# Kernel tuning notes

Measured on AMD Instinct MI355X. Metric: run time of the kernel, lower is better.

The kernel has to match this reference:

```python
import jax, jax.numpy as jnp
import numpy as np

N_EMBED = 512
E_DIM = 256
BETA = 0.25


def setup_inputs() -> dict:
    key = jax.random.key(0)
    k1, k2 = jax.random.split(key)
    z = jax.random.normal(k1, (32, 16, 16, 16, E_DIM), dtype=jnp.float32)
    embedding = jax.random.normal(k2, (N_EMBED, E_DIM), dtype=jnp.float32)
    return {"z": z, "embedding": embedding}


def reference(z, embedding):
    # Flatten spatial/batch dims: [N, e_dim]
    zf = z.reshape(-1, E_DIM)
    # similarity = ||z||^2 + ||e||^2 - 2 z.e  (squared distances)
    sim = (
        jnp.sum(zf * zf, axis=1, keepdims=True)
        + jnp.sum(embedding * embedding, axis=1)
        - 2.0 * jnp.einsum("bd,nd->bn", zf, embedding)
    )
    # NOTE: original code uses argmax (farthest code) -- faithfully reproduced.
    codebook_idxs = jnp.argmax(sim, axis=-1)
    # histogram side-effect: codebook_hist[idx] += 1
    hist = jnp.zeros((N_EMBED,), dtype=jnp.float32).at[codebook_idxs].add(1.0)
    z_q = embedding[codebook_idxs].reshape(z.shape)
    vq_loss = jnp.mean((z_q - jax.lax.stop_gradient(z)) ** 2)
    commitment_loss = BETA * jnp.mean((jax.lax.stop_gradient(z_q) - z) ** 2)
    # straight-through estimator
    z_q_st = z + jax.lax.stop_gradient(z_q - z)
    return (z_q_st, vq_loss, commitment_loss, codebook_idxs, hist)
```

## Files before the change

### kernel.cpp

```cpp
#include <hip/hip_runtime.h>
#include <hip/hip_bf16.h>

#define D 256
#define NC 512
#define NROWS 131072L

#define OFF_ZQ   0L
#define OFF_VQ   33554432L
#define OFF_CM   33554433L
#define OFF_IDX  33554434L
#define OFF_HIST 33685506L

#define WS_LPART 0
#define WS_HIST  2048
#define WS_E2    2560
#define WS_CNT   3072
#define WS_AMB   3136
#define WS_FIDX  134208
#define WS_BK    265280
#define WS_NEED  (330816L * 4)

#define MARGIN 1.25f

typedef __attribute__((ext_vector_type(8))) short bf16x8;
typedef __attribute__((ext_vector_type(4))) float f32x4;

#define AS1 __attribute__((address_space(1)))
#define AS3 __attribute__((address_space(3)))

__device__ __forceinline__ unsigned short f2bf(float f) {
    union { float f; unsigned int u; } a; a.f = f;
    return (unsigned short)((a.u + 0x7FFFu + ((a.u >> 16) & 1u)) >> 16);
}

__global__ void vq_init(float* __restrict__ ws) {
    int i = blockIdx.x * 1024 + threadIdx.x;
    if (i < 3073) ws[i] = 0.0f;
}

__global__ void vq_e2(const float* __restrict__ e, float* __restrict__ e2) {
    int c = blockIdx.x;
    int l = threadIdx.x;
    float4 v = *(const float4*)(e + c * D + l * 4);
    float s = v.x * v.x + v.y * v.y + v.z * v.z + v.w * v.w;
    #pragma unroll
    for (int off = 32; off; off >>= 1) s += __shfl_xor(s, off);
    if (l == 0) e2[c] = s;
}

__global__ void vq_convB(const float* __restrict__ e, unsigned short* __restrict__ Bk) {
    int code = blockIdx.x, k = threadIdx.x;
    unsigned short h = f2bf(e[code * D + k]);
    Bk[((k >> 5) * NC + code) * 32 + (k & 31)] = h;
}

__global__ __launch_bounds__(512, 4)
void vq_gemm(const float* __restrict__ z, const unsigned short* __restrict__ Bk,
             const float* __restrict__ e2, int* __restrict__ fidx,
             int* __restrict__ acnt, int* __restrict__ alist) {
    __shared__ __align__(16) unsigned short zh[64 * 264];
    __shared__ __align__(16) unsigned short Bs[512 * 32];
    __shared__ float red[64 * 4 * 3];

    const int tid = threadIdx.x;
    const int w = tid >> 6, l = tid & 63, q = l >> 4, ln = l & 15;
    const int wm = w >> 2, wn = w & 3;
    const long row0 = (long)blockIdx.x * 64;

    #pragma unroll
    for (int j = 0; j < 8; ++j) {
        int c = j * 512 + tid;
        int row = c >> 6, c4 = (c & 63) * 4;
        float4 av = *(const float4*)(z + (row0 + row) * D + c4);
        *(ushort4*)&zh[row * 264 + c4] =
            make_ushort4(f2bf(av.x), f2bf(av.y), f2bf(av.z), f2bf(av.w));
    }

    int bidx[8];
    #pragma unroll
    for (int nt = 0; nt < 8; ++nt) {
        int code = wn * 128 + nt * 16 + ln;
        int c = code * 4 + q;
        int d = c ^ ((code >> 1) & 3);
        bidx[nt] = d * 8;
    }

    f32x4 acc[2][8];
    #pragma unroll
    for (int mt = 0; mt < 2; ++mt)
        #pragma unroll
        for (int nt = 0; nt < 8; ++nt) acc[mt][nt] = (f32x4){0.f, 0.f, 0.f, 0.f};

    for (int s = 0; s < 8; ++s) {
        __syncthreads();
        const unsigned short* slabB = Bk + s * (NC * 32);
        #pragma unroll
        for (int j = 0; j < 4; ++j) {
            int dd = j * 512 + tid;
            int cc = dd ^ ((dd >> 3) & 3);
            __builtin_amdgcn_global_load_lds((const AS1 void*)(slabB + cc * 8),
                                             (AS3 void*)(Bs + dd * 8), 16, 0, 0);
        }
        __syncthreads();
        bf16x8 af[2], bfr[8];
        #pragma unroll
        for (int mt = 0; mt < 2; ++mt)
            af[mt] = *(const bf16x8*)&zh[(wm * 32 + mt * 16 + ln) * 264 + s * 32 + q * 8];
        #pragma unroll
        for (int nt = 0; nt < 8; ++nt)
            bfr[nt] = *(const bf16x8*)&Bs[bidx[nt]];
        #pragma unroll
        for (int mt = 0; mt < 2; ++mt)
            #pragma unroll
            for (int nt = 0; nt < 8; ++nt)
                acc[mt][nt] = __builtin_amdgcn_mfma_f32_16x16x32_bf16(af[mt], bfr[nt], acc[mt][nt], 0, 0, 0);
    }

    float e2v[8];
    #pragma unroll
    for (int nt = 0; nt < 8; ++nt) e2v[nt] = e2[wn * 128 + nt * 16 + ln];

    #pragma unroll
    for (int mt = 0; mt < 2; ++mt) {
        #pragma unroll
        for (int r = 0; r < 4; ++r) {
            float v1 = -3.0e38f, v2 = -3.0e38f; int i1 = 0;
            #pragma unroll
            for (int nt = 0; nt < 8; ++nt) {
                float v = e2v[nt] - 2.0f * acc[mt][nt][r];
                int c = wn * 128 + nt * 16 + ln;
                if (v > v1) { v2 = v1; v1 = v; i1 = c; }
                else if (v > v2) v2 = v;
            }
            #pragma unroll
            for (int off = 1; off < 16; off <<= 1) {
                float ov1 = __shfl_xor(v1, off);
                float ov2 = __shfl_xor(v2, off);
                int   oi1 = __shfl_xor(i1, off);
                if (ov1 > v1 || (ov1 == v1 && oi1 < i1)) {
                    v2 = fmaxf(v1, ov2); v1 = ov1; i1 = oi1;
                } else {
                    v2 = fmaxf(v2, ov1);
                }
            }
            if (ln == 0) {
                int rr = wm * 32 + mt * 16 + q * 4 + r;
                red[rr * 12 + wn * 3 + 0] = v1;
                red[rr * 12 + wn * 3 + 1] = (float)i1;
                red[rr * 12 + wn * 3 + 2] = v2;
            }
        }
    }
    __syncthreads();
    if (tid < 64) {
        float v1 = -3.0e38f, v2 = -3.0e38f; int i1 = 0;
        #pragma unroll
        for (int g = 0; g < 4; ++g) {
            float rv1 = red[tid * 12 + g * 3 + 0];
            int   ri  = (int)red[tid * 12 + g * 3 + 1];
            float rv2 = red[tid * 12 + g * 3 + 2];
            if (rv1 > v1) { v2 = fmaxf(v1, rv2); v1 = rv1; i1 = ri; }
            else v2 = fmaxf(v2, rv1);
        }
        fidx[row0 + tid] = i1;
        if (v1 - v2 < MARGIN) {
            int ppos = atomicAdd(acnt, 1);
            alist[ppos] = (int)(row0 + tid);
        }
    }
}

__global__ __launch_bounds__(256, 2)
void vq_refine(const float* __restrict__ z, const float* __restrict__ e,
               const float* __restrict__ e2, const int* __restrict__ acnt,
               const int* __restrict__ alist, int* __restrict__ fidx) {
    __shared__ __align__(16) float z_s[32][D];
    __shared__ __align__(16) float e_s[16][NC + 4];
    __shared__ int rowg[32];
    __shared__ int idx_s[32];
    const int tid = threadIdx.x, lane = tid & 63, w = tid >> 6;
    const int cnt = *acnt;
    for (int g = blockIdx.x; g * 32 < cnt; g += gridDim.x) {
        const int base = g * 32;
        __syncthreads();
        if (tid < 32) rowg[tid] = alist[min(base + tid, cnt - 1)];
        __syncthreads();
        #pragma unroll
        for (int j = 0; j < 8; ++j) {
            int c = j * 256 + tid, rl = c >> 6, c4 = (c & 63) * 4;
            *(float4*)&z_s[rl][c4] = *(const float4*)(z + (long)rowg[rl] * D + c4);
        }
        float acc[8][8];
        #pragma unroll
        for (int r = 0; r < 8; ++r)
            #pragma unroll
            for (int c = 0; c < 8; ++c) acc[r][c] = 0.0f;
        const int r0 = w * 8, c_lo = lane * 4;
        for (int kc = 0; kc < D; kc += 16) {
            __syncthreads();
            #pragma unroll
            for (int p = 0; p < 8; ++p) {
                int c = p * 64 + (tid >> 2), kk4 = (tid & 3) * 4;
                float4 v = *(const float4*)(e + c * D + kc + kk4);
                e_s[kk4 + 0][c] = v.x; e_s[kk4 + 1][c] = v.y;
                e_s[kk4 + 2][c] = v.z; e_s[kk4 + 3][c] = v.w;
            }
            __syncthreads();
            #pragma unroll
            for (int k4 = 0; k4 < 16; k4 += 4) {
                float zr[8][4];
                #pragma unroll
                for (int r = 0; r < 8; ++r) *(float4*)zr[r] = *(const float4*)&z_s[r0 + r][kc + k4];
                #pragma unroll
                for (int kk = 0; kk < 4; ++kk) {
                    float ev[8];
                    *(float4*)&ev[0] = *(const float4*)&e_s[k4 + kk][c_lo];
                    *(float4*)&ev[4] = *(const float4*)&e_s[k4 + kk][c_lo + 256];
                    #pragma unroll
                    for (int r = 0; r < 8; ++r)
                        #pragma unroll
                        for (int c = 0; c < 8; ++c) acc[r][c] = fmaf(zr[r][kk], ev[c], acc[r][c]);
                }
            }
        }
        float e2v[8];
        #pragma unroll
        for (int gg = 0; gg < 2; ++gg)
            #pragma unroll
            for (int i = 0; i < 4; ++i) e2v[gg * 4 + i] = e2[gg * 256 + c_lo + i];
        #pragma unroll
        for (int r = 0; r < 8; ++r) {
            float bvv = -3.0e38f; int bc = 0;
            #pragma unroll
            for (int c = 0; c < 8; ++c) {
                int col = (c >> 2) * 256 + c_lo + (c & 3);
                float v = e2v[c] - 2.0f * acc[r][c];
                if (v > bvv) { bvv = v; bc = col; }
            }
            #pragma unroll
            for (int off = 32; off; off >>= 1) {
                float ov = __shfl_xor(bvv, off); int oc = __shfl_xor(bc, off);
                if (ov > bvv || (ov == bvv && oc < bc)) { bvv = ov; bc = oc; }
            }
            if (lane == 0) idx_s[r0 + r] = bc;
        }
        __syncthreads();
        if (tid < 32 && base + tid < cnt) fidx[rowg[tid]] = idx_s[tid];
    }
}

__global__ __launch_bounds__(256)
void vq_hist(const int* __restrict__ fidx, float* __restrict__ out,
             float* __restrict__ hist) {
    __shared__ int h[NC];
    const int t = threadIdx.x;
    h[t] = 0; h[t + 256] = 0;
    __syncthreads();
    const long base = (long)blockIdx.x * 2048;
    #pragma unroll
    for (int j = 0; j < 8; ++j) {
        long i = base + j * 256 + t;
        int idx = fidx[i];
        out[OFF_IDX + i] = (float)idx;
        atomicAdd(&h[idx], 1);
    }
    __syncthreads();
    #pragma unroll
    for (int j = 0; j < 2; ++j) {
        int k = j * 256 + t;
        int c = h[k];
        if (c) atomicAdd(&hist[k], (float)c);
    }
}

__global__ __launch_bounds__(256)
void vq_epi(const float* __restrict__ z, const float* __restrict__ e,
            const int* __restrict__ fidx, float* __restrict__ out,
            float* __restrict__ lpart) {
    __shared__ int idxs[64];
    __shared__ float rs[4];
    const int t = threadIdx.x, lane = t & 63, w = t >> 6;
    const long row0 = (long)blockIdx.x * 64;
    if (t < 64) idxs[t] = fidx[row0 + t];
    __syncthreads();
    float ls = 0.f;
    #pragma unroll 4
    for (int j = 0; j < 16; ++j) {
        const int r = w * 16 + j;
        const long row = row0 + r;
        const int idx = idxs[r];
        float4 zv = *(const float4*)(z + row * D + lane * 4);
        float4 ev = *(const float4*)(e + (long)idx * D + lane * 4);
        float4 dq;
        dq.x = ev.x - zv.x; dq.y = ev.y - zv.y; dq.z = ev.z - zv.z; dq.w = ev.w - zv.w;
        float4 o;
        o.x = zv.x + dq.x; o.y = zv.y + dq.y; o.z = zv.z + dq.z; o.w = zv.w + dq.w;
        *(float4*)(out + OFF_ZQ + row * D + lane * 4) = o;
        ls += dq.x * dq.x + dq.y * dq.y + dq.z * dq.z + dq.w * dq.w;
    }
    #pragma unroll
    for (int off = 32; off; off >>= 1) ls += __shfl_xor(ls, off);
    if (lane == 0) rs[w] = ls;
    __syncthreads();
    if (t == 0) lpart[blockIdx.x] = rs[0] + rs[1] + rs[2] + rs[3];
}

__global__ void vq_fin(const float* __restrict__ ws, float* __restrict__ out) {
    __shared__ float sred[16];
    const int t = threadIdx.x, lane = t & 63, w = t >> 6;
    float s = ws[WS_LPART + t] + ws[WS_LPART + t + 1024];
    #pragma unroll
    for (int off = 32; off; off >>= 1) s += __shfl_xor(s, off);
    if (lane == 0) sred[w] = s;
    __syncthreads();
    if (t == 0) {
        float tot = 0.f;
        #pragma unroll
        for (int i = 0; i < 16; ++i) tot += sred[i];
        float m = tot / 33554432.0f;
        out[OFF_VQ] = m;
        out[OFF_CM] = 0.25f * m;
    }
    if (t < NC) out[OFF_HIST + t] = ws[WS_HIST + t];
}

__global__ __launch_bounds__(256, 2)
void vq_main_fb(const float* __restrict__ z, const float* __restrict__ e,
                const float* __restrict__ e2, float* __restrict__ out,
                float* __restrict__ ws_loss, float* __restrict__ ws_hist) {
    __shared__ __align__(16) float z_s[32][D];
    __shared__ __align__(16) float e_s[16][NC + 4];
    __shared__ int   idx_s[32];
    __shared__ float red_s[4];
    const int tid = threadIdx.x, lane = tid & 63, w = tid >> 6;
    const long row0 = (long)blockIdx.x * 32;
    {
        const float4* zg = (const float4*)(z + row0 * D);
        float4* zs = (float4*)(&z_s[0][0]);
        #pragma unroll
        for (int i = 0; i < 8; ++i) zs[i * 256 + tid] = zg[i * 256 + tid];
    }
    float acc[8][8];
    #pragma unroll
    for (int r = 0; r < 8; ++r)
        #pragma unroll
        for (int c = 0; c < 8; ++c) acc[r][c] = 0.0f;
    const int r0 = w * 8, c_lo = lane * 4;
    for (int kc = 0; kc < D; kc += 16) {
        __syncthreads();
        #pragma unroll
        for (int p = 0; p < 8; ++p) {
            int c = p * 64 + (tid >> 2), kk4 = (tid & 3) * 4;
            float4 v = *(const float4*)(e + c * D + kc + kk4);
            e_s[kk4 + 0][c] = v.x; e_s[kk4 + 1][c] = v.y;
            e_s[kk4 + 2][c] = v.z; e_s[kk4 + 3][c] = v.w;
        }
        __syncthreads();
        #pragma unroll
        for (int k4 = 0; k4 < 16; k4 += 4) {
            float zr[8][4];
            #pragma unroll
            for (int r = 0; r < 8; ++r) *(float4*)zr[r] = *(const float4*)&z_s[r0 + r][kc + k4];
            #pragma unroll
            for (int kk = 0; kk < 4; ++kk) {
                float ev[8];
                *(float4*)&ev[0] = *(const float4*)&e_s[k4 + kk][c_lo];
                *(float4*)&ev[4] = *(const float4*)&e_s[k4 + kk][c_lo + 256];
                #pragma unroll
                for (int r = 0; r < 8; ++r)
                    #pragma unroll
                    for (int c = 0; c < 8; ++c) acc[r][c] = fmaf(zr[r][kk], ev[c], acc[r][c]);
            }
        }
    }
    float e2v[8];
    #pragma unroll
    for (int g = 0; g < 2; ++g)
        #pragma unroll
        for (int i = 0; i < 4; ++i) e2v[g * 4 + i] = e2[g * 256 + c_lo + i];
    #pragma unroll
    for (int r = 0; r < 8; ++r) {
        float bvv = -3.0e38f; int bc = 0;
        #pragma unroll
        for (int c = 0; c < 8; ++c) {
            int col = (c >> 2) * 256 + c_lo + (c & 3);
            float v = e2v[c] - 2.0f * acc[r][c];
            if (v > bvv) { bvv = v; bc = col; }
        }
        #pragma unroll
        for (int off = 32; off; off >>= 1) {
            float ov = __shfl_xor(bvv, off); int oc = __shfl_xor(bc, off);
            if (ov > bvv || (ov == bvv && oc < bc)) { bvv = ov; bc = oc; }
        }
        if (lane == 0) idx_s[r0 + r] = bc;
    }
    __syncthreads();
    if (tid < 32) {
        int bc = idx_s[tid];
        out[OFF_IDX + row0 + tid] = (float)bc;
        atomicAdd(&ws_hist[bc], 1.0f);
    }
    float lsum = 0.0f;
    for (int r = 0; r < 32; ++r) {
        int idx = idx_s[r];
        float ev = e[idx * D + tid];
        float zv = z_s[r][tid];
        float dq = ev - zv;
        out[OFF_ZQ + (row0 + r) * D + tid] = zv + dq;
        lsum += dq * dq;
    }
    #pragma unroll
    for (int off = 32; off; off >>= 1) lsum += __shfl_xor(lsum, off);
    if (lane == 0) red_s[w] = lsum;
    __syncthreads();
    if (tid == 0) atomicAdd(ws_loss, red_s[0] + red_s[1] + red_s[2] + red_s[3]);
}

__global__ void vq_init_fb(float* __restrict__ ws) {
    int t = threadIdx.x;
    if (t < 513) ws[t] = 0.0f;
}
__global__ void vq_fin_fb(const float* __restrict__ ws, float* __restrict__ out) {
    int t = blockIdx.x * blockDim.x + threadIdx.x;
    if (t < NC) out[OFF_HIST + t] = ws[1 + t];
    if (t == NC) {
        float m = ws[0] / 33554432.0f;
        out[OFF_VQ] = m; out[OFF_CM] = 0.25f * m;
    }
}

extern "C" void kernel_launch(void* const* d_in, const int* in_sizes, int n_in,
                              void* d_out, int out_size, void* d_ws, size_t ws_size,
                              hipStream_t stream) {
    const float* z = (const float*)d_in[0];
    const float* e = (const float*)d_in[1];
    float* out = (float*)d_out;
    float* ws  = (float*)d_ws;

    if (ws_size >= (size_t)WS_NEED) {
        float* lpart = ws + WS_LPART;
        float* hist  = ws + WS_HIST;
        float* e2    = ws + WS_E2;
        int*   acnt  = (int*)(ws + WS_CNT);
        int*   alist = (int*)(ws + WS_AMB);
        int*   fidx  = (int*)(ws + WS_FIDX);
        unsigned short* Bk = (unsigned short*)(ws + WS_BK);

        vq_init<<<4, 1024, 0, stream>>>(ws);
        vq_e2<<<NC, 64, 0, stream>>>(e, e2);
        vq_convB<<<NC, 256, 0, stream>>>(e, Bk);
        vq_gemm<<<2048, 512, 0, stream>>>(z, Bk, e2, fidx, acnt, alist);
        vq_refine<<<512, 256, 0, stream>>>(z, e, e2, acnt, alist, fidx);
        vq_hist<<<64, 256, 0, stream>>>(fidx, out, hist);
        vq_epi<<<2048, 256, 0, stream>>>(z, e, fidx, out, lpart);
        vq_fin<<<1, 1024, 0, stream>>>(ws, out);
    } else {
        float* ws_loss = ws;
        float* ws_hist = ws + 1;
        float* ws_e2   = ws + 513;
        vq_init_fb<<<1, 1024, 0, stream>>>(ws);
        vq_e2<<<NC, 64, 0, stream>>>(e, ws_e2);
        vq_main_fb<<<4096, 256, 0, stream>>>(z, e, ws_e2, out, ws_loss, ws_hist);
        vq_fin_fb<<<3, 256, 0, stream>>>(ws, out);
    }
}
```

Before: 388.5 us.

## Fuse epilogue into GEMM, switch to fp16 MFMA, merge prep kernels

Switches the distance GEMM from bf16 to fp16 operands and tightens the ambiguity margin, so fewer rows go to the exact fp32 refine pass. It drops the LDS-staged B tiles: each wave now reads fp16 codebook fragments straight from global memory (L2-resident) for its own 64 codes. It fuses the z_q/loss epilogue into the GEMM for unambiguous rows and into the refine kernel for ambiguous rows, which removes a separate pass that re-read z. The init, e2 and conversion kernels are merged into one prep kernel. The tighter margin relies on fp16 precision being enough on these inputs, and direct global B loads may add latency.

```diff
diff --git a/kernel.cpp b/kernel.cpp
--- a/kernel.cpp
+++ b/kernel.cpp
@@ -12,123 +12,104 @@
 #define OFF_HIST 33685506L
 
 #define WS_LPART 0
-#define WS_HIST  2048
-#define WS_E2    2560
-#define WS_CNT   3072
-#define WS_AMB   3136
-#define WS_FIDX  134208
-#define WS_BK    265280
-#define WS_NEED  (330816L * 4)
-
-#define MARGIN 1.25f
-
-typedef __attribute__((ext_vector_type(8))) short bf16x8;
+#define WS_LOSSA 2048
+#define WS_HIST  2112
+#define WS_E2    2624
+#define WS_CNT   3136
+#define WS_AMB   3200
+#define WS_FIDX  134272
+#define WS_EF16  265344
+#define WS_NEED  (330880L * 4)
+
+#define MARGIN 0.125f
+
+typedef __attribute__((ext_vector_type(8))) _Float16 f16x8;
 typedef __attribute__((ext_vector_type(4))) float f32x4;
 
-#define AS1 __attribute__((address_space(1)))
-#define AS3 __attribute__((address_space(3)))
-
-__device__ __forceinline__ unsigned short f2bf(float f) {
-    union { float f; unsigned int u; } a; a.f = f;
-    return (unsigned short)((a.u + 0x7FFFu + ((a.u >> 16) & 1u)) >> 16);
-}
-
-__global__ void vq_init(float* __restrict__ ws) {
-    int i = blockIdx.x * 1024 + threadIdx.x;
-    if (i < 3073) ws[i] = 0.0f;
-}
-
-__global__ void vq_e2(const float* __restrict__ e, float* __restrict__ e2) {
-    int c = blockIdx.x;
-    int l = threadIdx.x;
-    float4 v = *(const float4*)(e + c * D + l * 4);
+__global__ void vq_prep(const float* __restrict__ e, float* __restrict__ ws) {
+    int c = blockIdx.x, t = threadIdx.x;
+    float4 v = *(const float4*)(e + c * D + t * 4);
     float s = v.x * v.x + v.y * v.y + v.z * v.z + v.w * v.w;
     #pragma unroll
     for (int off = 32; off; off >>= 1) s += __shfl_xor(s, off);
-    if (l == 0) e2[c] = s;
-}
-
-__global__ void vq_convB(const float* __restrict__ e, unsigned short* __restrict__ Bk) {
-    int code = blockIdx.x, k = threadIdx.x;
-    unsigned short h = f2bf(e[code * D + k]);
-    Bk[((k >> 5) * NC + code) * 32 + (k & 31)] = h;
+    if (t == 0) ws[WS_E2 + c] = s;
+    union { _Float16 h[4]; ushort4 u; } p;
+    p.h[0] = (_Float16)v.x; p.h[1] = (_Float16)v.y;
+    p.h[2] = (_Float16)v.z; p.h[3] = (_Float16)v.w;
+    unsigned short* ef16 = (unsigned short*)(ws + WS_EF16);
+    *(ushort4*)&ef16[c * D + t * 4] = p.u;
+    if (c == 0) {
+        #pragma unroll
+        for (int j = 0; j < 8; ++j) ws[WS_HIST + j * 64 + t] = 0.0f;
+        if (t == 0) { ((int*)(ws + WS_CNT))[0] = 0; ws[WS_LOSSA] = 0.0f; }
+    }
 }
 
 __global__ __launch_bounds__(512, 4)
-void vq_gemm(const float* __restrict__ z, const unsigned short* __restrict__ Bk,
-             const float* __restrict__ e2, int* __restrict__ fidx,
-             int* __restrict__ acnt, int* __restrict__ alist) {
+void vq_gemm(const float* __restrict__ z, const float* __restrict__ e,
+             const _Float16* __restrict__ ef16, const float* __restrict__ e2,
+             int* __restrict__ fidx, int* __restrict__ acnt, int* __restrict__ alist,
+             float* __restrict__ out, float* __restrict__ lpart) {
     __shared__ __align__(16) unsigned short zh[64 * 264];
-    __shared__ __align__(16) unsigned short Bs[512 * 32];
-    __shared__ float red[64 * 4 * 3];
+    __shared__ float red[64 * 8 * 3];
+    __shared__ int idx_s[64];
+    __shared__ int amb_s[64];
+    __shared__ float rs[8];
 
     const int tid = threadIdx.x;
     const int w = tid >> 6, l = tid & 63, q = l >> 4, ln = l & 15;
-    const int wm = w >> 2, wn = w & 3;
     const long row0 = (long)blockIdx.x * 64;
+    const float* zb = z + row0 * D;
 
     #pragma unroll
     for (int j = 0; j < 8; ++j) {
         int c = j * 512 + tid;
         int row = c >> 6, c4 = (c & 63) * 4;
-        float4 av = *(const float4*)(z + (row0 + row) * D + c4);
-        *(ushort4*)&zh[row * 264 + c4] =
-            make_ushort4(f2bf(av.x), f2bf(av.y), f2bf(av.z), f2bf(av.w));
-    }
-
-    int bidx[8];
-    #pragma unroll
-    for (int nt = 0; nt < 8; ++nt) {
-        int code = wn * 128 + nt * 16 + ln;
-        int c = code * 4 + q;
-        int d = c ^ ((code >> 1) & 3);
-        bidx[nt] = d * 8;
-    }
-
-    f32x4 acc[2][8];
-    #pragma unroll
-    for (int mt = 0; mt < 2; ++mt)
-        #pragma unroll
-        for (int nt = 0; nt < 8; ++nt) acc[mt][nt] = (f32x4){0.f, 0.f, 0.f, 0.f};
+        float4 av = *(const float4*)(zb + row * D + c4);
+        union { _Float16 h[4]; ushort4 u; } p;
+        p.h[0] = (_Float16)av.x; p.h[1] = (_Float16)av.y;
+        p.h[2] = (_Float16)av.z; p.h[3] = (_Float16)av.w;
+        *(ushort4*)&zh[row * 264 + c4] = p.u;
+    }
+    __syncthreads();
+
+    f32x4 acc[4][4];
+    #pragma unroll
+    for (int mt = 0; mt < 4; ++mt)
+        #pragma unroll
+        for (int nt = 0; nt < 4; ++nt) acc[mt][nt] = (f32x4){0.f, 0.f, 0.f, 0.f};
+
+    const _Float16* ebase = ef16 + (w * 64 + ln) * D + q * 8;
+    const _Float16* zh16 = (const _Float16*)zh;
 
     for (int s = 0; s < 8; ++s) {
-        __syncthreads();
-        const unsigned short* slabB = Bk + s * (NC * 32);
-        #pragma unroll
-        for (int j = 0; j < 4; ++j) {
-            int dd = j * 512 + tid;
-            int cc = dd ^ ((dd >> 3) & 3);
-            __builtin_amdgcn_global_load_lds((const AS1 void*)(slabB + cc * 8),
-                                             (AS3 void*)(Bs + dd * 8), 16, 0, 0);
-        }
-        __syncthreads();
-        bf16x8 af[2], bfr[8];
-        #pragma unroll
-        for (int mt = 0; mt < 2; ++mt)
-            af[mt] = *(const bf16x8*)&zh[(wm * 32 + mt * 16 + ln) * 264 + s * 32 + q * 8];
-        #pragma unroll
-        for (int nt = 0; nt < 8; ++nt)
-            bfr[nt] = *(const bf16x8*)&Bs[bidx[nt]];
-        #pragma unroll
-        for (int mt = 0; mt < 2; ++mt)
-            #pragma unroll
-            for (int nt = 0; nt < 8; ++nt)
-                acc[mt][nt] = __builtin_amdgcn_mfma_f32_16x16x32_bf16(af[mt], bfr[nt], acc[mt][nt], 0, 0, 0);
-    }
-
-    float e2v[8];
-    #pragma unroll
-    for (int nt = 0; nt < 8; ++nt) e2v[nt] = e2[wn * 128 + nt * 16 + ln];
-
-    #pragma unroll
-    for (int mt = 0; mt < 2; ++mt) {
+        f16x8 bfr[4], af[4];
+        #pragma unroll
+        for (int nt = 0; nt < 4; ++nt)
+            bfr[nt] = *(const f16x8*)(ebase + nt * 16 * D + s * 32);
+        #pragma unroll
+        for (int mt = 0; mt < 4; ++mt)
+            af[mt] = *(const f16x8*)&zh16[(mt * 16 + ln) * 264 + s * 32 + q * 8];
+        #pragma unroll
+        for (int mt = 0; mt < 4; ++mt)
+            #pragma unroll
+            for (int nt = 0; nt < 4; ++nt)
+                acc[mt][nt] = __builtin_amdgcn_mfma_f32_16x16x32_f16(af[mt], bfr[nt], acc[mt][nt], 0, 0, 0);
+    }
+
+    float e2v[4];
+    #pragma unroll
+    for (int nt = 0; nt < 4; ++nt) e2v[nt] = e2[w * 64 + nt * 16 + ln];
+
+    #pragma unroll
+    for (int mt = 0; mt < 4; ++mt) {
         #pragma unroll
         for (int r = 0; r < 4; ++r) {
             float v1 = -3.0e38f, v2 = -3.0e38f; int i1 = 0;
             #pragma unroll
-            for (int nt = 0; nt < 8; ++nt) {
+            for (int nt = 0; nt < 4; ++nt) {
                 float v = e2v[nt] - 2.0f * acc[mt][nt][r];
-                int c = wn * 128 + nt * 16 + ln;
+                int c = w * 64 + nt * 16 + ln;
                 if (v > v1) { v2 = v1; v1 = v; i1 = c; }
                 else if (v > v2) v2 = v;
             }
@@ -144,10 +125,10 @@
                 }
             }
             if (ln == 0) {
-                int rr = wm * 32 + mt * 16 + q * 4 + r;
-                red[rr * 12 + wn * 3 + 0] = v1;
-                red[rr * 12 + wn * 3 + 1] = (float)i1;
-                red[rr * 12 + wn * 3 + 2] = v2;
+                int rr = mt * 16 + q * 4 + r;
+                red[rr * 24 + w * 3 + 0] = v1;
+                red[rr * 24 + w * 3 + 1] = (float)i1;
+                red[rr * 24 + w * 3 + 2] = v2;
             }
         }
     }
@@ -155,31 +136,65 @@
     if (tid < 64) {
         float v1 = -3.0e38f, v2 = -3.0e38f; int i1 = 0;
         #pragma unroll
-        for (int g = 0; g < 4; ++g) {
-            float rv1 = red[tid * 12 + g * 3 + 0];
-            int   ri  = (int)red[tid * 12 + g * 3 + 1];
-            float rv2 = red[tid * 12 + g * 3 + 2];
+        for (int g = 0; g < 8; ++g) {
+            float rv1 = red[tid * 24 + g * 3 + 0];
+            int   ri  = (int)red[tid * 24 + g * 3 + 1];
+            float rv2 = red[tid * 24 + g * 3 + 2];
             if (rv1 > v1) { v2 = fmaxf(v1, rv2); v1 = rv1; i1 = ri; }
             else v2 = fmaxf(v2, rv1);
         }
+        idx_s[tid] = i1;
+        int amb = (v1 - v2 < MARGIN) ? 1 : 0;
+        amb_s[tid] = amb;
         fidx[row0 + tid] = i1;
-        if (v1 - v2 < MARGIN) {
-            int ppos = atomicAdd(acnt, 1);
-            alist[ppos] = (int)(row0 + tid);
-        }
+        if (amb) {
+            int p = atomicAdd(acnt, 1);
+            alist[p] = (int)(row0 + tid);
+        }
+    }
+    __syncthreads();
+
+    float ls = 0.f;
+    #pragma unroll
+    for (int j = 0; j < 8; ++j) {
+        int c = j * 512 + tid;
+        int rl = c >> 6, c4 = (c & 63) * 4;
+        if (!amb_s[rl]) {
+            int idx = idx_s[rl];
+            float4 zv = *(const float4*)(zb + rl * D + c4);
+            float4 ev = *(const float4*)(e + idx * D + c4);
+            float4 dq;
+            dq.x = ev.x - zv.x; dq.y = ev.y - zv.y; dq.z = ev.z - zv.z; dq.w = ev.w - zv.w;
+            float4 o;
+            o.x = zv.x + dq.x; o.y = zv.y + dq.y; o.z = zv.z + dq.z; o.w = zv.w + dq.w;
+            *(float4*)(out + OFF_ZQ + (row0 + rl) * D + c4) = o;
+            ls += dq.x * dq.x + dq.y * dq.y + dq.z * dq.z + dq.w * dq.w;
+        }
+    }
+    #pragma unroll
+    for (int off = 32; off; off >>= 1) ls += __shfl_xor(ls, off);
+    if (l == 0) rs[w] = ls;
+    __syncthreads();
+    if (tid == 0) {
+        float t = 0.f;
+        #pragma unroll
+        for (int i = 0; i < 8; ++i) t += rs[i];
+        lpart[blockIdx.x] = t;
     }
 }
 
 __global__ __launch_bounds__(256, 2)
 void vq_refine(const float* __restrict__ z, const float* __restrict__ e,
                const float* __restrict__ e2, const int* __restrict__ acnt,
-               const int* __restrict__ alist, int* __restrict__ fidx) {
+               const int* __restrict__ alist, int* __restrict__ fidx,
+               float* __restrict__ out, float* __restrict__ loss_amb) {
     __shared__ __align__(16) float z_s[32][D];
     __shared__ __align__(16) float e_s[16][NC + 4];
     __shared__ int rowg[32];
     __shared__ int idx_s[32];
     const int tid = threadIdx.x, lane = tid & 63, w = tid >> 6;
     const int cnt = *acnt;
+    float lacc = 0.f;
     for (int g = blockIdx.x; g * 32 < cnt; g += gridDim.x) {
         const int base = g * 32;
         __syncthreads();
@@ -246,6 +261,30 @@
         }
         __syncthreads();
         if (tid < 32 && base + tid < cnt) fidx[rowg[tid]] = idx_s[tid];
+        #pragma unroll
+        for (int j = 0; j < 8; ++j) {
+            int c = j * 256 + tid, rl = c >> 6, c4 = (c & 63) * 4;
+            if (base + rl < cnt) {
+                int idx = idx_s[rl];
+                float4 zv = *(const float4*)&z_s[rl][c4];
+                float4 ev = *(const float4*)(e + idx * D + c4);
+                float4 dq;
+                dq.x = ev.x - zv.x; dq.y = ev.y - zv.y; dq.z = ev.z - zv.z; dq.w = ev.w - zv.w;
+                float4 o;
+                o.x = zv.x + dq.x; o.y = zv.y + dq.y; o.z = zv.z + dq.z; o.w = zv.w + dq.w;
+                *(float4*)(out + OFF_ZQ + (long)rowg[rl] * D + c4) = o;
+                lacc += dq.x * dq.x + dq.y * dq.y + dq.z * dq.z + dq.w * dq.w;
+            }
+        }
+    }
+    #pragma unroll
+    for (int off = 32; off; off >>= 1) lacc += __shfl_xor(lacc, off);
+    __shared__ float rsum[4];
+    if (lane == 0) rsum[w] = lacc;
+    __syncthreads();
+    if (tid == 0) {
+        float t = rsum[0] + rsum[1] + rsum[2] + rsum[3];
+        if (t != 0.f) atomicAdd(loss_amb, t);
     }
 }
 
@@ -273,38 +312,6 @@
     }
 }
 
-__global__ __launch_bounds__(256)
-void vq_epi(const float* __restrict__ z, const float* __restrict__ e,
-            const int* __restrict__ fidx, float* __restrict__ out,
-            float* __restrict__ lpart) {
-    __shared__ int idxs[64];
-    __shared__ float rs[4];
-    const int t = threadIdx.x, lane = t & 63, w = t >> 6;
-    const long row0 = (long)blockIdx.x * 64;
-    if (t < 64) idxs[t] = fidx[row0 + t];
-    __syncthreads();
-    float ls = 0.f;
-    #pragma unroll 4
-    for (int j = 0; j < 16; ++j) {
-        const int r = w * 16 + j;
-        const long row = row0 + r;
-        const int idx = idxs[r];
-        float4 zv = *(const float4*)(z + row * D + lane * 4);
-        float4 ev = *(const float4*)(e + (long)idx * D + lane * 4);
-        float4 dq;
-        dq.x = ev.x - zv.x; dq.y = ev.y - zv.y; dq.z = ev.z - zv.z; dq.w = ev.w - zv.w;
-        float4 o;
-        o.x = zv.x + dq.x; o.y = zv.y + dq.y; o.z = zv.z + dq.z; o.w = zv.w + dq.w;
-        *(float4*)(out + OFF_ZQ + row * D + lane * 4) = o;
-        ls += dq.x * dq.x + dq.y * dq.y + dq.z * dq.z + dq.w * dq.w;
-    }
-    #pragma unroll
-    for (int off = 32; off; off >>= 1) ls += __shfl_xor(ls, off);
-    if (lane == 0) rs[w] = ls;
-    __syncthreads();
-    if (t == 0) lpart[blockIdx.x] = rs[0] + rs[1] + rs[2] + rs[3];
-}
-
 __global__ void vq_fin(const float* __restrict__ ws, float* __restrict__ out) {
     __shared__ float sred[16];
     const int t = threadIdx.x, lane = t & 63, w = t >> 6;
@@ -314,7 +321,7 @@
     if (lane == 0) sred[w] = s;
     __syncthreads();
     if (t == 0) {
-        float tot = 0.f;
+        float tot = ws[WS_LOSSA];
         #pragma unroll
         for (int i = 0; i < 16; ++i) tot += sred[i];
         float m = tot / 33554432.0f;
@@ -420,6 +427,14 @@
     int t = threadIdx.x;
     if (t < 513) ws[t] = 0.0f;
 }
+__global__ void vq_e2_fb(const float* __restrict__ e, float* __restrict__ e2) {
+    int c = blockIdx.x, l = threadIdx.x;
+    float4 v = *(const float4*)(e + c * D + l * 4);
+    float s = v.x * v.x + v.y * v.y + v.z * v.z + v.w * v.w;
+    #pragma unroll
+    for (int off = 32; off; off >>= 1) s += __shfl_xor(s, off);
+    if (l == 0) e2[c] = s;
+}
 __global__ void vq_fin_fb(const float* __restrict__ ws, float* __restrict__ out) {
     int t = blockIdx.x * blockDim.x + threadIdx.x;
     if (t < NC) out[OFF_HIST + t] = ws[1 + t];
@@ -439,27 +454,25 @@
 
     if (ws_size >= (size_t)WS_NEED) {
         float* lpart = ws + WS_LPART;
+        float* lossa = ws + WS_LOSSA;
         float* hist  = ws + WS_HIST;
         float* e2    = ws + WS_E2;
         int*   acnt  = (int*)(ws + WS_CNT);
         int*   alist = (int*)(ws + WS_AMB);
         int*   fidx  = (int*)(ws + WS_FIDX);
-        unsigned short* Bk = (unsigned short*)(ws + WS_BK);
-
-        vq_init<<<4, 1024, 0, stream>>>(ws);
-        vq_e2<<<NC, 64, 0, stream>>>(e, e2);
-        vq_convB<<<NC, 256, 0, stream>>>(e, Bk);
-        vq_gemm<<<2048, 512, 0, stream>>>(z, Bk, e2, fidx, acnt, alist);
-        vq_refine<<<512, 256, 0, stream>>>(z, e, e2, acnt, alist, fidx);
+        const _Float16* ef16 = (const _Float16*)(ws + WS_EF16);
+
+        vq_prep<<<NC, 64, 0, stream>>>(e, ws);
+        vq_gemm<<<2048, 512, 0, stream>>>(z, e, ef16, e2, fidx, acnt, alist, out, lpart);
+        vq_refine<<<512, 256, 0, stream>>>(z, e, e2, acnt, alist, fidx, out, lossa);
         vq_hist<<<64, 256, 0, stream>>>(fidx, out, hist);
-        vq_epi<<<2048, 256, 0, stream>>>(z, e, fidx, out, lpart);
         vq_fin<<<1, 1024, 0, stream>>>(ws, out);
     } else {
         float* ws_loss = ws;
         float* ws_hist = ws + 1;
         float* ws_e2   = ws + 513;
         vq_init_fb<<<1, 1024, 0, stream>>>(ws);
-        vq_e2<<<NC, 64, 0, stream>>>(e, ws_e2);
+        vq_e2_fb<<<NC, 64, 0, stream>>>(e, ws_e2);
         vq_main_fb<<<4096, 256, 0, stream>>>(z, e, ws_e2, out, ws_loss, ws_hist);
         vq_fin_fb<<<3, 256, 0, stream>>>(ws, out);
     }
```

Result: slower. 401.4 us (+3.3%).
